# Kernel optimization log

Measured on AMD Instinct MI355X. Metric: run time of the kernel, lower is better.

Reference implementation:

```python
import jax, jax.numpy as jnp
import numpy as np

B, N, DIM, H, DH = 8, 1024, 512, 8, 64
INNER = H * DH
SCALE = DH ** -0.5
EPS = 1e-12  # F.normalize eps


def setup_inputs() -> dict:
    key = jax.random.key(0)
    k1, k2, k3, k4, k5 = jax.random.split(key, 5)
    x = jax.random.normal(k1, (B, N, DIM), dtype=jnp.float32)
    spd = jax.random.normal(k2, (B, 1, N, N), dtype=jnp.float32)
    # per-head binomial keep mask (one realized draw of the original loop), guaranteed nonzero
    a = np.random.RandomState(0).binomial(1, 0.9, size=H)
    if a.sum() == 0:
        a[0] = 1
    head_mask = jnp.asarray(a, dtype=jnp.float32)
    W_qkv = jax.random.normal(k3, (DIM, 3 * INNER), dtype=jnp.float32) * (DIM ** -0.5)
    W_out = jax.random.normal(k4, (INNER, DIM), dtype=jnp.float32) * (INNER ** -0.5)
    b_out = jax.random.normal(k5, (DIM,), dtype=jnp.float32) * 0.01
    return {"x": x, "spd": spd, "head_mask": head_mask,
            "W_qkv": W_qkv, "W_out": W_out, "b_out": b_out}


def reference(x, spd, head_mask, W_qkv, W_out, b_out):
    b, n, _ = x.shape
    qkv = x @ W_qkv                                   # [b, n, 3*inner]
    q, k, v = jnp.split(qkv, 3, axis=-1)
    split_heads = lambda t: t.reshape(b, n, H, DH).transpose(0, 2, 1, 3)  # b h n d
    q, k, v = split_heads(q), split_heads(k), split_heads(v)

    dots = jnp.einsum('bhnd,bhmd->bhnm', q, k) * SCALE        # [b,h,n,n]
    prod = dots * spd                                         # broadcast spd over heads
    prod_norm = jnp.sqrt(jnp.sum(prod * prod, axis=-1, keepdims=True))
    dots_norm = jnp.sqrt(jnp.sum(dots * dots, axis=-1, keepdims=True))
    bias = prod / jnp.maximum(prod_norm, EPS) * dots_norm     # F.normalize(prod)*||dots||
    attn = jax.nn.softmax(dots + bias, axis=-1)

    # head dropout mask with rescale: attn * mask * H / sum(mask)
    scale_m = head_mask * (H / jnp.sum(head_mask))
    attn = attn * scale_m[None, :, None, None]

    out = jnp.einsum('bhnm,bhmd->bhnd', attn, v)              # [b,h,n,d]
    out = out.transpose(0, 2, 1, 3).reshape(b, n, INNER)      # b n (h d)
    return out @ W_out + b_out
```

## Files before the change

kernel.cpp:

```cpp
#include <hip/hip_runtime.h>
#include <hip/hip_bf16.h>

typedef __attribute__((ext_vector_type(8))) short short8;
typedef __attribute__((ext_vector_type(4))) short s16x4;
typedef __attribute__((ext_vector_type(4))) float f32x4;
typedef __attribute__((ext_vector_type(2))) _Float16 h2;

typedef const __attribute__((address_space(1))) unsigned* gp1;
typedef __attribute__((address_space(3))) unsigned* lp3;

__device__ inline short f2bf(float f) {
    union { float f; unsigned u; } v; v.f = f;
    unsigned r = v.u + 0x7fffu + ((v.u >> 16) & 1u);
    return (short)(r >> 16);
}

__global__ __launch_bounds__(256) void cvt_bf16(
    const float* __restrict__ src, short* __restrict__ dst, int n4)
{
    int i = blockIdx.x * 256 + threadIdx.x;
    if (i < n4) {
        float4 v = ((const float4*)src)[i];
        s16x4 o = { f2bf(v.x), f2bf(v.y), f2bf(v.z), f2bf(v.w) };
        ((s16x4*)dst)[i] = o;
    }
}

__global__ __launch_bounds__(256) void tr_w(
    const float* __restrict__ src, short* __restrict__ dst, int K, int N)
{
    __shared__ float t[64][65];
    const int k0 = blockIdx.x * 64, n0 = blockIdx.y * 64;
    const int r = threadIdx.x >> 4, c4 = (threadIdx.x & 15) * 4;
#pragma unroll
    for (int j = 0; j < 4; j++) {
        float4 v = *(const float4*)(src + (size_t)(k0 + r + 16 * j) * N + n0 + c4);
        t[r + 16 * j][c4 + 0] = v.x; t[r + 16 * j][c4 + 1] = v.y;
        t[r + 16 * j][c4 + 2] = v.z; t[r + 16 * j][c4 + 3] = v.w;
    }
    __syncthreads();
#pragma unroll
    for (int j = 0; j < 4; j++) {
        const int n = r + 16 * j;
        s16x4 o = { f2bf(t[c4 + 0][n]), f2bf(t[c4 + 1][n]),
                    f2bf(t[c4 + 2][n]), f2bf(t[c4 + 3][n]) };
        *(s16x4*)(dst + (size_t)(n0 + n) * K + k0 + c4) = o;
    }
}

__global__ __launch_bounds__(256) void qkv_gemm(
    const short* __restrict__ A, const short* __restrict__ BT,
    short* __restrict__ q, short* __restrict__ k, short* __restrict__ vt)
{
    __shared__ short sA[128][32];
    __shared__ short sB[128][32];

    const int tid  = threadIdx.x;
    const int wv   = tid >> 6, lane = tid & 63;
    const int quad = lane >> 4, l16 = lane & 15;
    const int wr = wv >> 1, wc = wv & 1;
    const int m0 = blockIdx.x * 128, n0 = blockIdx.y * 128;

    f32x4 acc[4][4];
#pragma unroll
    for (int i = 0; i < 4; i++)
#pragma unroll
        for (int j = 0; j < 4; j++) acc[i][j] = (f32x4){0.f, 0.f, 0.f, 0.f};

    const short* a_src = A  + (size_t)(m0 + wv * 32 + (lane >> 2)) * 512 + (lane & 3) * 8;
    const short* b_src = BT + (size_t)(n0 + wv * 32 + (lane >> 2)) * 512 + (lane & 3) * 8;
    char* a_dst = (char*)sA + wv * 2048;
    char* b_dst = (char*)sB + wv * 2048;

    for (int ks = 0; ks < 16; ks++) {
        __syncthreads();
        const short* ap = a_src + ks * 32;
        const short* bp = b_src + ks * 32;
        __builtin_amdgcn_global_load_lds((gp1)(ap),            (lp3)(a_dst),        16, 0, 0);
        __builtin_amdgcn_global_load_lds((gp1)(ap + 16 * 512), (lp3)(a_dst + 1024), 16, 0, 0);
        __builtin_amdgcn_global_load_lds((gp1)(bp),            (lp3)(b_dst),        16, 0, 0);
        __builtin_amdgcn_global_load_lds((gp1)(bp + 16 * 512), (lp3)(b_dst + 1024), 16, 0, 0);
        __syncthreads();

        short8 af[4], bf[4];
#pragma unroll
        for (int f = 0; f < 4; f++) {
            af[f] = *(const short8*)&sA[wr * 64 + f * 16 + l16][quad * 8];
            bf[f] = *(const short8*)&sB[wc * 64 + f * 16 + l16][quad * 8];
        }
#pragma unroll
        for (int fm = 0; fm < 4; fm++)
#pragma unroll
            for (int fn = 0; fn < 4; fn++)
                acc[fm][fn] = __builtin_amdgcn_mfma_f32_16x16x32_bf16(
                    af[fm], bf[fn], acc[fm][fn], 0, 0, 0);
    }

    const int sec = n0 >> 9;
#pragma unroll
    for (int fn = 0; fn < 4; fn++) {
        const int gc = n0 + wc * 64 + fn * 16 + l16;
        const int cc = gc & 511;
        const int h = cc >> 6, d = cc & 63;
#pragma unroll
        for (int fm = 0; fm < 4; fm++)
#pragma unroll
            for (int i = 0; i < 4; i++) {
                const int gm = m0 + wr * 64 + fm * 16 + quad * 4 + i;
                const int b = gm >> 10, n = gm & 1023;
                const int bh = b * 8 + h;
                if (sec == 0)      q[((size_t)(bh * 1024 + n)) * 64 + d] = f2bf(acc[fm][fn][i] * 0.125f);
                else if (sec == 1) k[((size_t)(bh * 1024 + n)) * 64 + d] = f2bf(acc[fm][fn][i]);
                else               vt[((size_t)(bh * 64 + d)) * 1024 + n] = f2bf(acc[fm][fn][i]);
            }
    }
}

__global__ __launch_bounds__(256, 3) void attn_k(
    const short* __restrict__ q, const short* __restrict__ kk,
    const short* __restrict__ vt, const float* __restrict__ spd,
    const float* __restrict__ hm, short* __restrict__ o)
{
    __shared__ short sP[16][1032];
    __shared__ float sred[4][4][16];

    const int tid  = threadIdx.x;
    const int wv   = tid >> 6, lane = tid & 63;
    const int quad = lane >> 4, l16 = lane & 15;
    const int qt = blockIdx.x, bh = blockIdx.y;
    const int b = bh >> 3, h = bh & 7;
    const int q0 = qt * 16;

    const short* qb = q + ((size_t)bh * 1024 + q0 + l16) * 64;
    short8 aq0 = *(const short8*)(qb + quad * 8);
    short8 aq1 = *(const short8*)(qb + 32 + quad * 8);

    f32x4 acc[16];
#pragma unroll
    for (int t = 0; t < 16; t++) acc[t] = (f32x4){0.f, 0.f, 0.f, 0.f};

    const short* kbh = kk + (size_t)bh * 1024 * 64;
    const float* spdb = spd + ((size_t)b * 1024 + q0 + quad * 4) * 1024;

    h2 svp[16][2];

    float svfA[8][4];
#pragma unroll
    for (int t = 0; t < 8; t++) {
        const float* sp = spdb + wv * 256 + t * 16 + l16;
        svfA[t][0] = sp[0];    svfA[t][1] = sp[1024];
        svfA[t][2] = sp[2048]; svfA[t][3] = sp[3072];
    }
#pragma unroll
    for (int t = 0; t < 8; t++) {
        const short* kb = kbh + (size_t)(wv * 256 + t * 16 + l16) * 64;
        short8 b0 = *(const short8*)(kb + quad * 8);
        short8 b1 = *(const short8*)(kb + 32 + quad * 8);
        acc[t] = __builtin_amdgcn_mfma_f32_16x16x32_bf16(aq0, b0, acc[t], 0, 0, 0);
        acc[t] = __builtin_amdgcn_mfma_f32_16x16x32_bf16(aq1, b1, acc[t], 0, 0, 0);
    }
#pragma unroll
    for (int t = 0; t < 8; t++) {
        svp[t][0] = (h2){(_Float16)svfA[t][0], (_Float16)svfA[t][1]};
        svp[t][1] = (h2){(_Float16)svfA[t][2], (_Float16)svfA[t][3]};
    }
    float svfB[8][4];
#pragma unroll
    for (int t = 0; t < 8; t++) {
        const float* sp = spdb + wv * 256 + (t + 8) * 16 + l16;
        svfB[t][0] = sp[0];    svfB[t][1] = sp[1024];
        svfB[t][2] = sp[2048]; svfB[t][3] = sp[3072];
    }
#pragma unroll
    for (int t = 8; t < 16; t++) {
        const short* kb = kbh + (size_t)(wv * 256 + t * 16 + l16) * 64;
        short8 b0 = *(const short8*)(kb + quad * 8);
        short8 b1 = *(const short8*)(kb + 32 + quad * 8);
        acc[t] = __builtin_amdgcn_mfma_f32_16x16x32_bf16(aq0, b0, acc[t], 0, 0, 0);
        acc[t] = __builtin_amdgcn_mfma_f32_16x16x32_bf16(aq1, b1, acc[t], 0, 0, 0);
    }
#pragma unroll
    for (int t = 0; t < 8; t++) {
        svp[t + 8][0] = (h2){(_Float16)svfB[t][0], (_Float16)svfB[t][1]};
        svp[t + 8][1] = (h2){(_Float16)svfB[t][2], (_Float16)svfB[t][3]};
    }

    float dn[4] = {0.f, 0.f, 0.f, 0.f}, pn[4] = {0.f, 0.f, 0.f, 0.f};
#pragma unroll
    for (int t = 0; t < 16; t++)
#pragma unroll
        for (int i = 0; i < 4; i++) {
            float s  = acc[t][i];
            float sv = (float)svp[t][i >> 1][i & 1];
            float ps = s * sv;
            dn[i] += s * s;
            pn[i] += ps * ps;
        }
#pragma unroll
    for (int m = 1; m < 16; m <<= 1)
#pragma unroll
        for (int i = 0; i < 4; i++) {
            dn[i] += __shfl_xor(dn[i], m, 64);
            pn[i] += __shfl_xor(pn[i], m, 64);
        }
    if (l16 == 0)
#pragma unroll
        for (int i = 0; i < 4; i++) {
            sred[0][wv][quad * 4 + i] = dn[i];
            sred[1][wv][quad * 4 + i] = pn[i];
        }
    __syncthreads();
    float ratio[4];
#pragma unroll
    for (int i = 0; i < 4; i++) {
        const int row = quad * 4 + i;
        float d = sred[0][0][row] + sred[0][1][row] + sred[0][2][row] + sred[0][3][row];
        float p = sred[1][0][row] + sred[1][1][row] + sred[1][2][row] + sred[1][3][row];
        ratio[i] = sqrtf(d) / fmaxf(sqrtf(p), 1e-12f);
    }

    float mx[4] = {-1e30f, -1e30f, -1e30f, -1e30f};
#pragma unroll
    for (int t = 0; t < 16; t++)
#pragma unroll
        for (int i = 0; i < 4; i++) {
            float s  = acc[t][i];
            float sv = (float)svp[t][i >> 1][i & 1];
            float l  = s * fmaf(sv, ratio[i], 1.0f);
            acc[t][i] = l;
            mx[i] = fmaxf(mx[i], l);
        }
#pragma unroll
    for (int m = 1; m < 16; m <<= 1)
#pragma unroll
        for (int i = 0; i < 4; i++) mx[i] = fmaxf(mx[i], __shfl_xor(mx[i], m, 64));
    if (l16 == 0)
#pragma unroll
        for (int i = 0; i < 4; i++) sred[2][wv][quad * 4 + i] = mx[i];
    __syncthreads();
    float mrow[4];
#pragma unroll
    for (int i = 0; i < 4; i++) {
        const int row = quad * 4 + i;
        mrow[i] = fmaxf(fmaxf(sred[2][0][row], sred[2][1][row]),
                        fmaxf(sred[2][2][row], sred[2][3][row]));
    }

    float rs[4] = {0.f, 0.f, 0.f, 0.f};
#pragma unroll
    for (int t = 0; t < 16; t++)
#pragma unroll
        for (int i = 0; i < 4; i++) {
            float p = __expf(acc[t][i] - mrow[i]);
            acc[t][i] = p;
            rs[i] += p;
        }
#pragma unroll
    for (int m = 1; m < 16; m <<= 1)
#pragma unroll
        for (int i = 0; i < 4; i++) rs[i] += __shfl_xor(rs[i], m, 64);
    if (l16 == 0)
#pragma unroll
        for (int i = 0; i < 4; i++) sred[3][wv][quad * 4 + i] = rs[i];
    __syncthreads();
    const float hsum = hm[0] + hm[1] + hm[2] + hm[3] + hm[4] + hm[5] + hm[6] + hm[7];
    const float hscale = hm[h] * 8.0f / hsum;
    float rinv[4];
#pragma unroll
    for (int i = 0; i < 4; i++) {
        const int row = quad * 4 + i;
        float s = sred[3][0][row] + sred[3][1][row] + sred[3][2][row] + sred[3][3][row];
        rinv[i] = hscale / s;
    }

#pragma unroll
    for (int t = 0; t < 16; t++) {
        const int col = wv * 256 + t * 16 + l16;
#pragma unroll
        for (int i = 0; i < 4; i++)
            sP[quad * 4 + i][col] = f2bf(acc[t][i] * rinv[i]);
    }
    __syncthreads();

    f32x4 oacc = (f32x4){0.f, 0.f, 0.f, 0.f};
    const short* vb = vt + ((size_t)bh * 64 + wv * 16 + l16) * 1024;
#pragma unroll
    for (int kkk = 0; kkk < 32; kkk++) {
        short8 pa = *(const short8*)&sP[l16][kkk * 32 + quad * 8];
        short8 vf = *(const short8*)(vb + kkk * 32 + quad * 8);
        oacc = __builtin_amdgcn_mfma_f32_16x16x32_bf16(pa, vf, oacc, 0, 0, 0);
    }
#pragma unroll
    for (int i = 0; i < 4; i++)
        o[((size_t)(b * 1024 + q0 + quad * 4 + i)) * 512 + h * 64 + wv * 16 + l16]
            = f2bf(oacc[i]);
}

__global__ __launch_bounds__(256) void out_gemm(
    const short* __restrict__ A, const short* __restrict__ BT,
    const float* __restrict__ bias, float* __restrict__ out)
{
    __shared__ short sA[128][32];
    __shared__ short sB[128][32];

    const int tid  = threadIdx.x;
    const int wv   = tid >> 6, lane = tid & 63;
    const int quad = lane >> 4, l16 = lane & 15;
    const int wr = wv >> 1, wc = wv & 1;
    const int m0 = blockIdx.x * 128, n0 = blockIdx.y * 128;

    f32x4 acc[4][4];
#pragma unroll
    for (int i = 0; i < 4; i++)
#pragma unroll
        for (int j = 0; j < 4; j++) acc[i][j] = (f32x4){0.f, 0.f, 0.f, 0.f};

    const short* a_src = A  + (size_t)(m0 + wv * 32 + (lane >> 2)) * 512 + (lane & 3) * 8;
    const short* b_src = BT + (size_t)(n0 + wv * 32 + (lane >> 2)) * 512 + (lane & 3) * 8;
    char* a_dst = (char*)sA + wv * 2048;
    char* b_dst = (char*)sB + wv * 2048;

    for (int ks = 0; ks < 16; ks++) {
        __syncthreads();
        const short* ap = a_src + ks * 32;
        const short* bp = b_src + ks * 32;
        __builtin_amdgcn_global_load_lds((gp1)(ap),            (lp3)(a_dst),        16, 0, 0);
        __builtin_amdgcn_global_load_lds((gp1)(ap + 16 * 512), (lp3)(a_dst + 1024), 16, 0, 0);
        __builtin_amdgcn_global_load_lds((gp1)(bp),            (lp3)(b_dst),        16, 0, 0);
        __builtin_amdgcn_global_load_lds((gp1)(bp + 16 * 512), (lp3)(b_dst + 1024), 16, 0, 0);
        __syncthreads();

        short8 af[4], bf[4];
#pragma unroll
        for (int f = 0; f < 4; f++) {
            af[f] = *(const short8*)&sA[wr * 64 + f * 16 + l16][quad * 8];
            bf[f] = *(const short8*)&sB[wc * 64 + f * 16 + l16][quad * 8];
        }
#pragma unroll
        for (int fm = 0; fm < 4; fm++)
#pragma unroll
            for (int fn = 0; fn < 4; fn++)
                acc[fm][fn] = __builtin_amdgcn_mfma_f32_16x16x32_bf16(
                    af[fm], bf[fn], acc[fm][fn], 0, 0, 0);
    }

#pragma unroll
    for (int fn = 0; fn < 4; fn++) {
        const int gc = n0 + wc * 64 + fn * 16 + l16;
        const float bv = bias[gc];
#pragma unroll
        for (int fm = 0; fm < 4; fm++)
#pragma unroll
            for (int i = 0; i < 4; i++) {
                const int gm = m0 + wr * 64 + fm * 16 + quad * 4 + i;
                out[(size_t)gm * 512 + gc] = acc[fm][fn][i] + bv;
            }
    }
}

extern "C" void kernel_launch(void* const* d_in, const int* in_sizes, int n_in,
                              void* d_out, int out_size, void* d_ws, size_t ws_size,
                              hipStream_t stream) {
    const float* x    = (const float*)d_in[0];
    const float* spd  = (const float*)d_in[1];
    const float* hm   = (const float*)d_in[2];
    const float* Wqkv = (const float*)d_in[3];
    const float* Wout = (const float*)d_in[4];
    const float* bout = (const float*)d_in[5];
    float* out = (float*)d_out;

    char* ws = (char*)d_ws;
    short* qw  = (short*)(ws);
    short* kw  = (short*)(ws + ((size_t)8  << 20));
    short* vtw = (short*)(ws + ((size_t)16 << 20));
    short* ow  = (short*)(ws + ((size_t)24 << 20));
    short* xb  = (short*)(ws + ((size_t)32 << 20));
    short* wqT = (short*)(ws + ((size_t)40 << 20));
    short* woT = (short*)(ws + ((size_t)42 << 20));

    cvt_bf16<<<4096, 256, 0, stream>>>(x, xb, 8192 * 512 / 4);
    tr_w    <<<dim3(8, 24), 256, 0, stream>>>(Wqkv, wqT, 512, 1536);
    tr_w    <<<dim3(8, 8),  256, 0, stream>>>(Wout, woT, 512, 512);

    qkv_gemm<<<dim3(64, 12), 256, 0, stream>>>(xb, wqT, qw, kw, vtw);
    attn_k  <<<dim3(64, 64), 256, 0, stream>>>(qw, kw, vtw, spd, hm, ow);
    out_gemm<<<dim3(64, 4),  256, 0, stream>>>(ow, woT, bout, out);
}
```

Baseline: 276.0 us.

## Pre-convert spd to fp16, async-load into LDS, drop softmax max pass

Adds a pre-pass that converts the spd matrix to fp16 once, so the attention kernel reads half the bytes per head instead of re-reading fp32 spd. Each block streams its spd rows straight into the shared P buffer with global_load_lds while the QK MFMAs run. The V transpose moves from scattered stores in the QKV GEMM epilogue into a separate tiled transpose kernel. The softmax max-reduction pass and one barrier are removed, exponentiating logits directly, which risks overflow for large logits. Occupancy hint rises from 3 to 4 blocks.

```diff
diff --git a/kernel.cpp b/kernel.cpp
--- a/kernel.cpp
+++ b/kernel.cpp
@@ -4,7 +4,6 @@
 typedef __attribute__((ext_vector_type(8))) short short8;
 typedef __attribute__((ext_vector_type(4))) short s16x4;
 typedef __attribute__((ext_vector_type(4))) float f32x4;
-typedef __attribute__((ext_vector_type(2))) _Float16 h2;
 
 typedef const __attribute__((address_space(1))) unsigned* gp1;
 typedef __attribute__((address_space(3))) unsigned* lp3;
@@ -13,6 +12,12 @@
     union { float f; unsigned u; } v; v.f = f;
     unsigned r = v.u + 0x7fffu + ((v.u >> 16) & 1u);
     return (short)(r >> 16);
+}
+__device__ inline short f2h(float f) {
+    union { _Float16 h; short s; } u; u.h = (_Float16)f; return u.s;
+}
+__device__ inline float h2f(short s) {
+    union { short s; _Float16 h; } u; u.s = s; return (float)u.h;
 }
 
 __global__ __launch_bounds__(256) void cvt_bf16(
@@ -26,6 +31,17 @@
     }
 }
 
+__global__ __launch_bounds__(256) void cvt_f16(
+    const float* __restrict__ src, short* __restrict__ dst, int n4)
+{
+    int i = blockIdx.x * 256 + threadIdx.x;
+    if (i < n4) {
+        float4 v = ((const float4*)src)[i];
+        s16x4 o = { f2h(v.x), f2h(v.y), f2h(v.z), f2h(v.w) };
+        ((s16x4*)dst)[i] = o;
+    }
+}
+
 __global__ __launch_bounds__(256) void tr_w(
     const float* __restrict__ src, short* __restrict__ dst, int K, int N)
 {
@@ -48,9 +64,29 @@
     }
 }
 
+__global__ __launch_bounds__(256) void tv(
+    const short* __restrict__ v, short* __restrict__ vt)
+{
+    __shared__ short t[64][72];
+    const int nt = blockIdx.x, bh = blockIdx.y;
+    const int r = threadIdx.x >> 2, seg = (threadIdx.x & 3) * 16;
+    const short* src = v + ((size_t)(bh * 1024 + nt * 64 + r)) * 64 + seg;
+    *(short8*)&t[r][seg]     = *(const short8*)src;
+    *(short8*)&t[r][seg + 8] = *(const short8*)(src + 8);
+    __syncthreads();
+    short8 a, c;
+#pragma unroll
+    for (int j = 0; j < 8; j++) a[j] = t[seg + j][r];
+#pragma unroll
+    for (int j = 0; j < 8; j++) c[j] = t[seg + 8 + j][r];
+    short* dst = vt + ((size_t)(bh * 64 + r)) * 1024 + nt * 64 + seg;
+    *(short8*)dst = a;
+    *(short8*)(dst + 8) = c;
+}
+
 __global__ __launch_bounds__(256) void qkv_gemm(
     const short* __restrict__ A, const short* __restrict__ BT,
-    short* __restrict__ q, short* __restrict__ k, short* __restrict__ vt)
+    short* __restrict__ q, short* __restrict__ k, short* __restrict__ vv)
 {
     __shared__ short sA[128][32];
     __shared__ short sB[128][32];
@@ -109,20 +145,20 @@
                 const int gm = m0 + wr * 64 + fm * 16 + quad * 4 + i;
                 const int b = gm >> 10, n = gm & 1023;
                 const int bh = b * 8 + h;
-                if (sec == 0)      q[((size_t)(bh * 1024 + n)) * 64 + d] = f2bf(acc[fm][fn][i] * 0.125f);
-                else if (sec == 1) k[((size_t)(bh * 1024 + n)) * 64 + d] = f2bf(acc[fm][fn][i]);
-                else               vt[((size_t)(bh * 64 + d)) * 1024 + n] = f2bf(acc[fm][fn][i]);
+                if (sec == 0)      q[((size_t)(bh * 1024 + n)) * 64 + d]  = f2bf(acc[fm][fn][i] * 0.125f);
+                else if (sec == 1) k[((size_t)(bh * 1024 + n)) * 64 + d]  = f2bf(acc[fm][fn][i]);
+                else               vv[((size_t)(bh * 1024 + n)) * 64 + d] = f2bf(acc[fm][fn][i]);
             }
     }
 }
 
-__global__ __launch_bounds__(256, 3) void attn_k(
+__global__ __launch_bounds__(256, 4) void attn_k(
     const short* __restrict__ q, const short* __restrict__ kk,
-    const short* __restrict__ vt, const float* __restrict__ spd,
+    const short* __restrict__ vt, const short* __restrict__ spd16,
     const float* __restrict__ hm, short* __restrict__ o)
 {
     __shared__ short sP[16][1032];
-    __shared__ float sred[4][4][16];
+    __shared__ float sred[3][4][16];
 
     const int tid  = threadIdx.x;
     const int wv   = tid >> 6, lane = tid & 63;
@@ -131,6 +167,17 @@
     const int b = bh >> 3, h = bh & 7;
     const int q0 = qt * 16;
 
+    {
+        const short* base = spd16 + ((size_t)b * 1024 + q0) * 1024;
+#pragma unroll
+        for (int i2 = 0; i2 < 8; i2++) {
+            const int row = wv * 4 + (i2 >> 1), half = i2 & 1;
+            const short* gp = base + (size_t)row * 1024 + half * 512 + lane * 8;
+            __builtin_amdgcn_global_load_lds(
+                (gp1)gp, (lp3)((char*)&sP[0][0] + row * 2064 + half * 1024), 16, 0, 0);
+        }
+    }
+
     const short* qb = q + ((size_t)bh * 1024 + q0 + l16) * 64;
     short8 aq0 = *(const short8*)(qb + quad * 8);
     short8 aq1 = *(const short8*)(qb + 32 + quad * 8);
@@ -140,62 +187,29 @@
     for (int t = 0; t < 16; t++) acc[t] = (f32x4){0.f, 0.f, 0.f, 0.f};
 
     const short* kbh = kk + (size_t)bh * 1024 * 64;
-    const float* spdb = spd + ((size_t)b * 1024 + q0 + quad * 4) * 1024;
-
-    h2 svp[16][2];
-
-    float svfA[8][4];
-#pragma unroll
-    for (int t = 0; t < 8; t++) {
-        const float* sp = spdb + wv * 256 + t * 16 + l16;
-        svfA[t][0] = sp[0];    svfA[t][1] = sp[1024];
-        svfA[t][2] = sp[2048]; svfA[t][3] = sp[3072];
-    }
-#pragma unroll
-    for (int t = 0; t < 8; t++) {
+#pragma unroll
+    for (int t = 0; t < 16; t++) {
         const short* kb = kbh + (size_t)(wv * 256 + t * 16 + l16) * 64;
         short8 b0 = *(const short8*)(kb + quad * 8);
         short8 b1 = *(const short8*)(kb + 32 + quad * 8);
         acc[t] = __builtin_amdgcn_mfma_f32_16x16x32_bf16(aq0, b0, acc[t], 0, 0, 0);
         acc[t] = __builtin_amdgcn_mfma_f32_16x16x32_bf16(aq1, b1, acc[t], 0, 0, 0);
     }
-#pragma unroll
-    for (int t = 0; t < 8; t++) {
-        svp[t][0] = (h2){(_Float16)svfA[t][0], (_Float16)svfA[t][1]};
-        svp[t][1] = (h2){(_Float16)svfA[t][2], (_Float16)svfA[t][3]};
-    }
-    float svfB[8][4];
-#pragma unroll
-    for (int t = 0; t < 8; t++) {
-        const float* sp = spdb + wv * 256 + (t + 8) * 16 + l16;
-        svfB[t][0] = sp[0];    svfB[t][1] = sp[1024];
-        svfB[t][2] = sp[2048]; svfB[t][3] = sp[3072];
-    }
-#pragma unroll
-    for (int t = 8; t < 16; t++) {
-        const short* kb = kbh + (size_t)(wv * 256 + t * 16 + l16) * 64;
-        short8 b0 = *(const short8*)(kb + quad * 8);
-        short8 b1 = *(const short8*)(kb + 32 + quad * 8);
-        acc[t] = __builtin_amdgcn_mfma_f32_16x16x32_bf16(aq0, b0, acc[t], 0, 0, 0);
-        acc[t] = __builtin_amdgcn_mfma_f32_16x16x32_bf16(aq1, b1, acc[t], 0, 0, 0);
-    }
-#pragma unroll
-    for (int t = 0; t < 8; t++) {
-        svp[t + 8][0] = (h2){(_Float16)svfB[t][0], (_Float16)svfB[t][1]};
-        svp[t + 8][1] = (h2){(_Float16)svfB[t][2], (_Float16)svfB[t][3]};
-    }
+    __syncthreads();
 
     float dn[4] = {0.f, 0.f, 0.f, 0.f}, pn[4] = {0.f, 0.f, 0.f, 0.f};
 #pragma unroll
-    for (int t = 0; t < 16; t++)
+    for (int t = 0; t < 16; t++) {
+        const int col = wv * 256 + t * 16 + l16;
 #pragma unroll
         for (int i = 0; i < 4; i++) {
             float s  = acc[t][i];
-            float sv = (float)svp[t][i >> 1][i & 1];
+            float sv = h2f(sP[quad * 4 + i][col]);
             float ps = s * sv;
             dn[i] += s * s;
             pn[i] += ps * ps;
         }
+    }
 #pragma unroll
     for (int m = 1; m < 16; m <<= 1)
 #pragma unroll
@@ -219,49 +233,26 @@
         ratio[i] = sqrtf(d) / fmaxf(sqrtf(p), 1e-12f);
     }
 
-    float mx[4] = {-1e30f, -1e30f, -1e30f, -1e30f};
-#pragma unroll
-    for (int t = 0; t < 16; t++)
+    float rs[4] = {0.f, 0.f, 0.f, 0.f};
+#pragma unroll
+    for (int t = 0; t < 16; t++) {
+        const int col = wv * 256 + t * 16 + l16;
 #pragma unroll
         for (int i = 0; i < 4; i++) {
-            float s  = acc[t][i];
-            float sv = (float)svp[t][i >> 1][i & 1];
-            float l  = s * fmaf(sv, ratio[i], 1.0f);
-            acc[t][i] = l;
-            mx[i] = fmaxf(mx[i], l);
-        }
-#pragma unroll
-    for (int m = 1; m < 16; m <<= 1)
-#pragma unroll
-        for (int i = 0; i < 4; i++) mx[i] = fmaxf(mx[i], __shfl_xor(mx[i], m, 64));
-    if (l16 == 0)
-#pragma unroll
-        for (int i = 0; i < 4; i++) sred[2][wv][quad * 4 + i] = mx[i];
-    __syncthreads();
-    float mrow[4];
-#pragma unroll
-    for (int i = 0; i < 4; i++) {
-        const int row = quad * 4 + i;
-        mrow[i] = fmaxf(fmaxf(sred[2][0][row], sred[2][1][row]),
-                        fmaxf(sred[2][2][row], sred[2][3][row]));
-    }
-
-    float rs[4] = {0.f, 0.f, 0.f, 0.f};
-#pragma unroll
-    for (int t = 0; t < 16; t++)
-#pragma unroll
-        for (int i = 0; i < 4; i++) {
-            float p = __expf(acc[t][i] - mrow[i]);
+            float sv = h2f(sP[quad * 4 + i][col]);
+            float l  = acc[t][i] * fmaf(sv, ratio[i], 1.0f);
+            float p  = __expf(l);
             acc[t][i] = p;
             rs[i] += p;
         }
+    }
 #pragma unroll
     for (int m = 1; m < 16; m <<= 1)
 #pragma unroll
         for (int i = 0; i < 4; i++) rs[i] += __shfl_xor(rs[i], m, 64);
     if (l16 == 0)
 #pragma unroll
-        for (int i = 0; i < 4; i++) sred[3][wv][quad * 4 + i] = rs[i];
+        for (int i = 0; i < 4; i++) sred[2][wv][quad * 4 + i] = rs[i];
     __syncthreads();
     const float hsum = hm[0] + hm[1] + hm[2] + hm[3] + hm[4] + hm[5] + hm[6] + hm[7];
     const float hscale = hm[h] * 8.0f / hsum;
@@ -269,7 +260,7 @@
 #pragma unroll
     for (int i = 0; i < 4; i++) {
         const int row = quad * 4 + i;
-        float s = sred[3][0][row] + sred[3][1][row] + sred[3][2][row] + sred[3][3][row];
+        float s = sred[2][0][row] + sred[2][1][row] + sred[2][2][row] + sred[2][3][row];
         rinv[i] = hscale / s;
     }
 
@@ -370,19 +361,23 @@
     float* out = (float*)d_out;
 
     char* ws = (char*)d_ws;
-    short* qw  = (short*)(ws);
-    short* kw  = (short*)(ws + ((size_t)8  << 20));
-    short* vtw = (short*)(ws + ((size_t)16 << 20));
-    short* ow  = (short*)(ws + ((size_t)24 << 20));
-    short* xb  = (short*)(ws + ((size_t)32 << 20));
-    short* wqT = (short*)(ws + ((size_t)40 << 20));
-    short* woT = (short*)(ws + ((size_t)42 << 20));
+    short* qw   = (short*)(ws);
+    short* kw   = (short*)(ws + ((size_t)8  << 20));
+    short* vw   = (short*)(ws + ((size_t)16 << 20));
+    short* vtw  = (short*)(ws + ((size_t)24 << 20));
+    short* ow   = (short*)(ws + ((size_t)32 << 20));
+    short* xb   = (short*)(ws + ((size_t)40 << 20));
+    short* wqT  = (short*)(ws + ((size_t)48 << 20));
+    short* woT  = (short*)(ws + ((size_t)50 << 20));
+    short* spdh = (short*)(ws + ((size_t)52 << 20));
 
     cvt_bf16<<<4096, 256, 0, stream>>>(x, xb, 8192 * 512 / 4);
+    cvt_f16 <<<8192, 256, 0, stream>>>(spd, spdh, 8 * 1024 * 1024 / 4);
     tr_w    <<<dim3(8, 24), 256, 0, stream>>>(Wqkv, wqT, 512, 1536);
     tr_w    <<<dim3(8, 8),  256, 0, stream>>>(Wout, woT, 512, 512);
 
-    qkv_gemm<<<dim3(64, 12), 256, 0, stream>>>(xb, wqT, qw, kw, vtw);
-    attn_k  <<<dim3(64, 64), 256, 0, stream>>>(qw, kw, vtw, spd, hm, ow);
+    qkv_gemm<<<dim3(64, 12), 256, 0, stream>>>(xb, wqT, qw, kw, vw);
+    tv      <<<dim3(16, 64), 256, 0, stream>>>(vw, vtw);
+    attn_k  <<<dim3(64, 64), 256, 0, stream>>>(qw, kw, vtw, spdh, hm, ow);
     out_gemm<<<dim3(64, 4),  256, 0, stream>>>(ow, woT, bout, out);
 }
```

Result: slower. 284.8 us (+3.2%).
